# Performance work log

Measured on AMD Instinct MI355X. Metric: run time of the kernel, lower is better.

Reference implementation:

```python
import jax, jax.numpy as jnp
import numpy as np

B, S, H, L = 64, 2048, 1024, 15


def setup_inputs() -> dict:
    key = jax.random.key(0)
    ks = jax.random.split(key, 16)
    x = jax.random.normal(ks[0], (B, S, H), dtype=jnp.float32)
    # valid spans: start in [1, S-40), length in [1, 32)
    s1 = jax.random.randint(ks[1], (B,), 1, S - 40)
    l1 = jax.random.randint(ks[2], (B,), 1, 32)
    s2 = jax.random.randint(ks[3], (B,), 1, S - 40)
    l2 = jax.random.randint(ks[4], (B,), 1, 32)
    entity_idx = jnp.stack([s1, s1 + l1, s2, s2 + l2], axis=1).astype(jnp.int32)
    sc = 1.0 / np.sqrt(H)
    W_cls = jax.random.normal(ks[5], (H, H), jnp.float32) * sc
    b_cls = jnp.zeros((H,), jnp.float32)
    W_e1 = jax.random.normal(ks[6], (H, H), jnp.float32) * sc
    b_e1 = jnp.zeros((H,), jnp.float32)
    W_e2 = jax.random.normal(ks[7], (H, H), jnp.float32) * sc
    b_e2 = jnp.zeros((H,), jnp.float32)
    W1 = jax.random.normal(ks[8], (3 * H, H), jnp.float32) * (1.0 / np.sqrt(3 * H))
    b1 = jnp.zeros((H,), jnp.float32)
    W2 = jax.random.normal(ks[9], (H, H), jnp.float32) * sc
    b2 = jnp.zeros((H,), jnp.float32)
    Wout = jax.random.normal(ks[10], (H, L), jnp.float32) * sc
    bout = jnp.zeros((L,), jnp.float32)
    return {"x": x, "entity_idx": entity_idx, "W_cls": W_cls, "b_cls": b_cls,
            "W_e1": W_e1, "b_e1": b_e1, "W_e2": W_e2, "b_e2": b_e2,
            "W1": W1, "b1": b1, "W2": W2, "b2": b2, "Wout": Wout, "bout": bout}


def _span_mean(x, start, end):
    # x: [B,S,H]; start,end: [B] int -> masked mean over [start,end)
    pos = jnp.arange(x.shape[1])[None, :]  # [1,S]
    mask = ((pos >= start[:, None]) & (pos < end[:, None])).astype(x.dtype)  # [B,S]
    cnt = jnp.maximum(mask.sum(axis=1, keepdims=True), 1.0)  # [B,1]
    return jnp.einsum('bs,bsh->bh', mask, x) / cnt


def reference(x, entity_idx, W_cls, b_cls, W_e1, b_e1, W_e2, b_e2,
              W1, b1, W2, b2, Wout, bout):
    subj = _span_mean(x, entity_idx[:, 0], entity_idx[:, 1])  # [B,H]
    obj = _span_mean(x, entity_idx[:, 2], entity_idx[:, 3])   # [B,H]
    x0 = jnp.tanh(x[:, 0, :]) @ W_cls + b_cls
    e1 = jnp.tanh(subj) @ W_e1 + b_e1
    e2 = jnp.tanh(obj) @ W_e2 + b_e2
    h = jnp.concatenate([x0, e1, e2], axis=1)  # [B,3H]
    h = h @ W1 + b1           # dropout is identity at eval
    h = h @ W2 + b2
    out = h @ Wout + bout     # [B,num_labels]
    return out
```

## Files before the change

kernel.cpp:

```cpp
#include <hip/hip_runtime.h>
#include <math.h>

#define BB 64
#define SS 2048
#define HH 1024
#define LL 15

__global__ void span_tanh_kernel(const float* __restrict__ x,
                                 const int* __restrict__ eidx,
                                 float* __restrict__ t_cat,
                                 float* __restrict__ h_cat,
                                 float* __restrict__ h1,
                                 float* __restrict__ h2) {
  int b = blockIdx.x;
  int part = blockIdx.y;
  int tid = threadIdx.x;
  int h4 = tid * 4;
  const float* xb = x + (size_t)b * SS * HH;
  float* tb = t_cat + (size_t)b * 3 * HH;
  const float4 zero4 = {0.f, 0.f, 0.f, 0.f};

  if (part == 0) {
    float4* z = (float4*)(h_cat + (size_t)b * 3 * HH);
    z[tid] = zero4; z[tid + 256] = zero4; z[tid + 512] = zero4;

    int s1 = eidx[b * 4 + 0], e1 = eidx[b * 4 + 1];
    float c1 = (float)max(e1 - s1, 1);
    float4 v0 = *(const float4*)&xb[h4];
    float4 a = zero4;
    for (int s = s1; s < e1; ++s) {
      float4 v = *(const float4*)&xb[(size_t)s * HH + h4];
      a.x += v.x; a.y += v.y; a.z += v.z; a.w += v.w;
    }
    float4 o0 = {tanhf(v0.x), tanhf(v0.y), tanhf(v0.z), tanhf(v0.w)};
    *(float4*)&tb[h4] = o0;
    float4 o1 = {tanhf(a.x / c1), tanhf(a.y / c1), tanhf(a.z / c1), tanhf(a.w / c1)};
    *(float4*)&tb[HH + h4] = o1;
  } else {
    ((float4*)(h1 + (size_t)b * HH))[tid] = zero4;
    ((float4*)(h2 + (size_t)b * HH))[tid] = zero4;

    int s2 = eidx[b * 4 + 2], e2 = eidx[b * 4 + 3];
    float c2 = (float)max(e2 - s2, 1);
    float4 a = zero4;
    for (int s = s2; s < e2; ++s) {
      float4 v = *(const float4*)&xb[(size_t)s * HH + h4];
      a.x += v.x; a.y += v.y; a.z += v.z; a.w += v.w;
    }
    float4 o2 = {tanhf(a.x / c2), tanhf(a.y / c2), tanhf(a.z / c2), tanhf(a.w / c2)};
    *(float4*)&tb[2 * HH + h4] = o2;
  }
}

#define LSTR 68
__device__ __forceinline__ void gemm_tile_body(
    const float* __restrict__ A, int lda,
    const float* __restrict__ W, int ldw,
    const float* __restrict__ bias,
    float* __restrict__ C, int ldc,
    int k0, int kend, int j0, bool addBias) {
  __shared__ float As[32 * LSTR];
  __shared__ float Ws[32 * LSTR];
  int tid = threadIdx.x;
  int tx = tid & 15, ty = tid >> 4;

  float4 aReg[2], wReg[2];
  int aRow[2], aKq[2], wRow[2], wCq[2];
#pragma unroll
  for (int i = 0; i < 2; ++i) {
    int idx = tid + i * 256;
    aRow[i] = idx & 63; aKq[i] = idx >> 6;
    wRow[i] = idx >> 4; wCq[i] = idx & 15;
  }

  auto loadRegs = [&](int kb) {
#pragma unroll
    for (int i = 0; i < 2; ++i) {
      aReg[i] = *(const float4*)&A[(size_t)aRow[i] * lda + kb + 4 * aKq[i]];
      wReg[i] = *(const float4*)&W[(size_t)(kb + wRow[i]) * ldw + j0 + 4 * wCq[i]];
    }
  };

  float acc[4][4] = {{0.f}};
  loadRegs(k0);
  for (int kb = k0; kb < kend; kb += 32) {
#pragma unroll
    for (int i = 0; i < 2; ++i) {
      float av[4] = {aReg[i].x, aReg[i].y, aReg[i].z, aReg[i].w};
#pragma unroll
      for (int j = 0; j < 4; ++j) As[(4 * aKq[i] + j) * LSTR + aRow[i]] = av[j];
      *(float4*)&Ws[wRow[i] * LSTR + 4 * wCq[i]] = wReg[i];
    }
    __syncthreads();
    if (kb + 32 < kend) loadRegs(kb + 32);
#pragma unroll
    for (int kk = 0; kk < 32; ++kk) {
      float4 a4 = *(const float4*)&As[kk * LSTR + ty * 4];
      float4 w4 = *(const float4*)&Ws[kk * LSTR + tx * 4];
      float a[4] = {a4.x, a4.y, a4.z, a4.w};
      float w[4] = {w4.x, w4.y, w4.z, w4.w};
#pragma unroll
      for (int i = 0; i < 4; ++i)
#pragma unroll
        for (int j = 0; j < 4; ++j) acc[i][j] += a[i] * w[j];
    }
    __syncthreads();
  }
#pragma unroll
  for (int i = 0; i < 4; ++i) {
    int r = ty * 4 + i;
#pragma unroll
    for (int j = 0; j < 4; ++j) {
      int c = j0 + tx * 4 + j;
      float v = acc[i][j];
      if (addBias) v += bias[c];
      atomicAdd(&C[(size_t)r * ldc + c], v);
    }
  }
}

__global__ void gemm_bd_kernel(const float* __restrict__ t_cat,
                               const float* __restrict__ Wc, const float* __restrict__ bc,
                               const float* __restrict__ We1, const float* __restrict__ be1,
                               const float* __restrict__ We2, const float* __restrict__ be2,
                               float* __restrict__ h_cat, int Kchunk) {
  int z = blockIdx.z;
  const float* W = (z == 0) ? Wc : ((z == 1) ? We1 : We2);
  const float* bias = (z == 0) ? bc : ((z == 1) ? be1 : be2);
  const float* A = t_cat + z * HH;
  float* C = h_cat + z * HH;
  int k0 = blockIdx.y * Kchunk;
  gemm_tile_body(A, 3 * HH, W, HH, bias, C, 3 * HH,
                 k0, k0 + Kchunk, blockIdx.x * 64, blockIdx.y == 0);
}

__global__ void gemm_kernel(const float* __restrict__ A, int lda,
                            const float* __restrict__ W, int ldw,
                            const float* __restrict__ bias,
                            float* __restrict__ C, int ldc, int Kchunk) {
  int k0 = blockIdx.y * Kchunk;
  gemm_tile_body(A, lda, W, ldw, bias, C, ldc,
                 k0, k0 + Kchunk, blockIdx.x * 64, blockIdx.y == 0);
}

__global__ void out_kernel(const float* __restrict__ h2,
                           const float* __restrict__ Wout,
                           const float* __restrict__ bout,
                           float* __restrict__ out) {
  int tid = threadIdx.x;
  int lane = tid & 63;
  int idx = blockIdx.x * 4 + (tid >> 6);
  int b = idx / LL, l = idx % LL;
  const float* h = h2 + (size_t)b * HH;
  float acc = 0.f;
#pragma unroll
  for (int w = 0; w < 4; ++w) {
    int k0 = (w * 64 + lane) * 4;
    float4 h4 = *(const float4*)&h[k0];
    acc += h4.x * Wout[(size_t)(k0 + 0) * LL + l];
    acc += h4.y * Wout[(size_t)(k0 + 1) * LL + l];
    acc += h4.z * Wout[(size_t)(k0 + 2) * LL + l];
    acc += h4.w * Wout[(size_t)(k0 + 3) * LL + l];
  }
#pragma unroll
  for (int off = 32; off > 0; off >>= 1) acc += __shfl_down(acc, off, 64);
  if (lane == 0) out[idx] = acc + bout[l];
}

extern "C" void kernel_launch(void* const* d_in, const int* in_sizes, int n_in,
                              void* d_out, int out_size, void* d_ws, size_t ws_size,
                              hipStream_t stream) {
  const float* x     = (const float*)d_in[0];
  const int*   eidx  = (const int*)d_in[1];
  const float* W_cls = (const float*)d_in[2];
  const float* b_cls = (const float*)d_in[3];
  const float* W_e1  = (const float*)d_in[4];
  const float* b_e1  = (const float*)d_in[5];
  const float* W_e2  = (const float*)d_in[6];
  const float* b_e2  = (const float*)d_in[7];
  const float* W1    = (const float*)d_in[8];
  const float* b1    = (const float*)d_in[9];
  const float* W2    = (const float*)d_in[10];
  const float* b2    = (const float*)d_in[11];
  const float* Wout  = (const float*)d_in[12];
  const float* bout  = (const float*)d_in[13];
  float* out = (float*)d_out;

  float* ws    = (float*)d_ws;
  float* t_cat = ws;
  float* h_cat = t_cat + BB * 3 * HH;
  float* h1    = h_cat + BB * 3 * HH;
  float* h2    = h1 + BB * HH;

  span_tanh_kernel<<<dim3(BB, 2), 256, 0, stream>>>(x, eidx, t_cat, h_cat, h1, h2);

  gemm_bd_kernel<<<dim3(16, 8, 3), 256, 0, stream>>>(
      t_cat, W_cls, b_cls, W_e1, b_e1, W_e2, b_e2, h_cat, 128);

  gemm_kernel<<<dim3(16, 24, 1), 256, 0, stream>>>(h_cat, 3 * HH, W1, HH, b1, h1, HH, 128);

  gemm_kernel<<<dim3(16, 16, 1), 256, 0, stream>>>(h1, HH, W2, HH, b2, h2, HH, 64);

  out_kernel<<<dim3(240), 256, 0, stream>>>(h2, Wout, bout, out);
}
```

Measured before the change: 718.7 us.

## Fuse all stages into one cooperative persistent kernel with grid syncs

Replaces five separate kernel launches with a single cooperative kernel of 512 blocks that runs the span pooling, three GEMM stages and the output projection, separated by grid-wide syncs. The split-K factors change: the W1 GEMM now uses 32 K-chunks of 96 and the W2 GEMM 32 chunks of 32, so more blocks run in those stages. The aim is to remove launch gaps and make better use of the GPU for the small GEMMs. In exchange it adds grid.sync overhead, more atomicAdd contention from the finer split-K, and a cooperative launch whose return value is never checked.

```diff
diff --git a/kernel.cpp b/kernel.cpp
--- a/kernel.cpp
+++ b/kernel.cpp
@@ -1,58 +1,16 @@
 #include <hip/hip_runtime.h>
+#include <hip/hip_cooperative_groups.h>
 #include <math.h>
 
 #define BB 64
 #define SS 2048
 #define HH 1024
 #define LL 15
-
-__global__ void span_tanh_kernel(const float* __restrict__ x,
-                                 const int* __restrict__ eidx,
-                                 float* __restrict__ t_cat,
-                                 float* __restrict__ h_cat,
-                                 float* __restrict__ h1,
-                                 float* __restrict__ h2) {
-  int b = blockIdx.x;
-  int part = blockIdx.y;
-  int tid = threadIdx.x;
-  int h4 = tid * 4;
-  const float* xb = x + (size_t)b * SS * HH;
-  float* tb = t_cat + (size_t)b * 3 * HH;
-  const float4 zero4 = {0.f, 0.f, 0.f, 0.f};
-
-  if (part == 0) {
-    float4* z = (float4*)(h_cat + (size_t)b * 3 * HH);
-    z[tid] = zero4; z[tid + 256] = zero4; z[tid + 512] = zero4;
-
-    int s1 = eidx[b * 4 + 0], e1 = eidx[b * 4 + 1];
-    float c1 = (float)max(e1 - s1, 1);
-    float4 v0 = *(const float4*)&xb[h4];
-    float4 a = zero4;
-    for (int s = s1; s < e1; ++s) {
-      float4 v = *(const float4*)&xb[(size_t)s * HH + h4];
-      a.x += v.x; a.y += v.y; a.z += v.z; a.w += v.w;
-    }
-    float4 o0 = {tanhf(v0.x), tanhf(v0.y), tanhf(v0.z), tanhf(v0.w)};
-    *(float4*)&tb[h4] = o0;
-    float4 o1 = {tanhf(a.x / c1), tanhf(a.y / c1), tanhf(a.z / c1), tanhf(a.w / c1)};
-    *(float4*)&tb[HH + h4] = o1;
-  } else {
-    ((float4*)(h1 + (size_t)b * HH))[tid] = zero4;
-    ((float4*)(h2 + (size_t)b * HH))[tid] = zero4;
-
-    int s2 = eidx[b * 4 + 2], e2 = eidx[b * 4 + 3];
-    float c2 = (float)max(e2 - s2, 1);
-    float4 a = zero4;
-    for (int s = s2; s < e2; ++s) {
-      float4 v = *(const float4*)&xb[(size_t)s * HH + h4];
-      a.x += v.x; a.y += v.y; a.z += v.z; a.w += v.w;
-    }
-    float4 o2 = {tanhf(a.x / c2), tanhf(a.y / c2), tanhf(a.z / c2), tanhf(a.w / c2)};
-    *(float4*)&tb[2 * HH + h4] = o2;
-  }
-}
-
+#define NBLK 512
 #define LSTR 68
+
+namespace cg = cooperative_groups;
+
 __device__ __forceinline__ void gemm_tile_body(
     const float* __restrict__ A, int lda,
     const float* __restrict__ W, int ldw,
@@ -119,52 +77,111 @@
   }
 }
 
-__global__ void gemm_bd_kernel(const float* __restrict__ t_cat,
-                               const float* __restrict__ Wc, const float* __restrict__ bc,
-                               const float* __restrict__ We1, const float* __restrict__ be1,
-                               const float* __restrict__ We2, const float* __restrict__ be2,
-                               float* __restrict__ h_cat, int Kchunk) {
-  int z = blockIdx.z;
-  const float* W = (z == 0) ? Wc : ((z == 1) ? We1 : We2);
-  const float* bias = (z == 0) ? bc : ((z == 1) ? be1 : be2);
-  const float* A = t_cat + z * HH;
-  float* C = h_cat + z * HH;
-  int k0 = blockIdx.y * Kchunk;
-  gemm_tile_body(A, 3 * HH, W, HH, bias, C, 3 * HH,
-                 k0, k0 + Kchunk, blockIdx.x * 64, blockIdx.y == 0);
-}
-
-__global__ void gemm_kernel(const float* __restrict__ A, int lda,
-                            const float* __restrict__ W, int ldw,
-                            const float* __restrict__ bias,
-                            float* __restrict__ C, int ldc, int Kchunk) {
-  int k0 = blockIdx.y * Kchunk;
-  gemm_tile_body(A, lda, W, ldw, bias, C, ldc,
-                 k0, k0 + Kchunk, blockIdx.x * 64, blockIdx.y == 0);
-}
-
-__global__ void out_kernel(const float* __restrict__ h2,
-                           const float* __restrict__ Wout,
-                           const float* __restrict__ bout,
-                           float* __restrict__ out) {
+__global__ void fused_kernel(const float* __restrict__ x,
+                             const int* __restrict__ eidx,
+                             const float* __restrict__ W_cls, const float* __restrict__ b_cls,
+                             const float* __restrict__ W_e1,  const float* __restrict__ b_e1,
+                             const float* __restrict__ W_e2,  const float* __restrict__ b_e2,
+                             const float* __restrict__ W1,    const float* __restrict__ b1,
+                             const float* __restrict__ W2,    const float* __restrict__ b2,
+                             const float* __restrict__ Wout,  const float* __restrict__ bout,
+                             float* __restrict__ out,
+                             float* __restrict__ t_cat,
+                             float* __restrict__ h_cat,
+                             float* __restrict__ h1,
+                             float* __restrict__ h2) {
+  cg::grid_group grid = cg::this_grid();
+  int blk = blockIdx.x;
   int tid = threadIdx.x;
-  int lane = tid & 63;
-  int idx = blockIdx.x * 4 + (tid >> 6);
-  int b = idx / LL, l = idx % LL;
-  const float* h = h2 + (size_t)b * HH;
-  float acc = 0.f;
-#pragma unroll
-  for (int w = 0; w < 4; ++w) {
-    int k0 = (w * 64 + lane) * 4;
-    float4 h4 = *(const float4*)&h[k0];
-    acc += h4.x * Wout[(size_t)(k0 + 0) * LL + l];
-    acc += h4.y * Wout[(size_t)(k0 + 1) * LL + l];
-    acc += h4.z * Wout[(size_t)(k0 + 2) * LL + l];
-    acc += h4.w * Wout[(size_t)(k0 + 3) * LL + l];
-  }
-#pragma unroll
-  for (int off = 32; off > 0; off >>= 1) acc += __shfl_down(acc, off, 64);
-  if (lane == 0) out[idx] = acc + bout[l];
+
+  {
+    const float4 zero4 = {0.f, 0.f, 0.f, 0.f};
+    int zidx = blk * 256 + tid;
+    if (zidx < (BB * 5 * HH) / 4) ((float4*)h_cat)[zidx] = zero4;
+
+    if (blk < 2 * BB) {
+      int b = blk & 63;
+      int part = blk >> 6;
+      int h4 = tid * 4;
+      const float* xb = x + (size_t)b * SS * HH;
+      float* tb = t_cat + (size_t)b * 3 * HH;
+      if (part == 0) {
+        int s1 = eidx[b * 4 + 0], e1 = eidx[b * 4 + 1];
+        float c1 = (float)max(e1 - s1, 1);
+        float4 v0 = *(const float4*)&xb[h4];
+        float4 a = zero4;
+        for (int s = s1; s < e1; ++s) {
+          float4 v = *(const float4*)&xb[(size_t)s * HH + h4];
+          a.x += v.x; a.y += v.y; a.z += v.z; a.w += v.w;
+        }
+        float4 o0 = {tanhf(v0.x), tanhf(v0.y), tanhf(v0.z), tanhf(v0.w)};
+        *(float4*)&tb[h4] = o0;
+        float4 o1 = {tanhf(a.x / c1), tanhf(a.y / c1), tanhf(a.z / c1), tanhf(a.w / c1)};
+        *(float4*)&tb[HH + h4] = o1;
+      } else {
+        int s2 = eidx[b * 4 + 2], e2 = eidx[b * 4 + 3];
+        float c2 = (float)max(e2 - s2, 1);
+        float4 a = zero4;
+        for (int s = s2; s < e2; ++s) {
+          float4 v = *(const float4*)&xb[(size_t)s * HH + h4];
+          a.x += v.x; a.y += v.y; a.z += v.z; a.w += v.w;
+        }
+        float4 o2 = {tanhf(a.x / c2), tanhf(a.y / c2), tanhf(a.z / c2), tanhf(a.w / c2)};
+        *(float4*)&tb[2 * HH + h4] = o2;
+      }
+    }
+  }
+  grid.sync();
+
+  if (blk < 384) {
+    int jcol = blk & 15;
+    int rest = blk >> 4;
+    int ks = rest & 7;
+    int z = rest >> 3;
+    const float* W = (z == 0) ? W_cls : ((z == 1) ? W_e1 : W_e2);
+    const float* bias = (z == 0) ? b_cls : ((z == 1) ? b_e1 : b_e2);
+    gemm_tile_body(t_cat + z * HH, 3 * HH, W, HH, bias, h_cat + z * HH, 3 * HH,
+                   ks * 128, ks * 128 + 128, jcol * 64, ks == 0);
+  }
+  grid.sync();
+
+  {
+    int jcol = blk & 15;
+    int ks = blk >> 4;
+    gemm_tile_body(h_cat, 3 * HH, W1, HH, b1, h1, HH,
+                   ks * 96, ks * 96 + 96, jcol * 64, ks == 0);
+  }
+  grid.sync();
+
+  {
+    int jcol = blk & 15;
+    int ks = blk >> 4;
+    gemm_tile_body(h1, HH, W2, HH, b2, h2, HH,
+                   ks * 32, ks * 32 + 32, jcol * 64, ks == 0);
+  }
+  grid.sync();
+
+  {
+    int lane = tid & 63;
+    int idx = blk * 4 + (tid >> 6);
+    if (idx < BB * LL) {
+      int b = idx / LL, l = idx % LL;
+      const float* h = h2 + (size_t)b * HH;
+      float acc = 0.f;
+#pragma unroll
+      for (int w = 0; w < 4; ++w) {
+        int k0 = (w * 64 + lane) * 4;
+        float4 hv = *(const float4*)&h[k0];
+        acc += hv.x * Wout[(size_t)(k0 + 0) * LL + l];
+        acc += hv.y * Wout[(size_t)(k0 + 1) * LL + l];
+        acc += hv.z * Wout[(size_t)(k0 + 2) * LL + l];
+        acc += hv.w * Wout[(size_t)(k0 + 3) * LL + l];
+      }
+#pragma unroll
+      for (int off = 32; off > 0; off >>= 1) acc += __shfl_down(acc, off, 64);
+      if (lane == 0) out[idx] = acc + bout[l];
+    }
+  }
 }
 
 extern "C" void kernel_launch(void* const* d_in, const int* in_sizes, int n_in,
@@ -192,14 +209,12 @@
   float* h1    = h_cat + BB * 3 * HH;
   float* h2    = h1 + BB * HH;
 
-  span_tanh_kernel<<<dim3(BB, 2), 256, 0, stream>>>(x, eidx, t_cat, h_cat, h1, h2);
-
-  gemm_bd_kernel<<<dim3(16, 8, 3), 256, 0, stream>>>(
-      t_cat, W_cls, b_cls, W_e1, b_e1, W_e2, b_e2, h_cat, 128);
-
-  gemm_kernel<<<dim3(16, 24, 1), 256, 0, stream>>>(h_cat, 3 * HH, W1, HH, b1, h1, HH, 128);
-
-  gemm_kernel<<<dim3(16, 16, 1), 256, 0, stream>>>(h1, HH, W2, HH, b2, h2, HH, 64);
-
-  out_kernel<<<dim3(240), 256, 0, stream>>>(h2, Wout, bout, out);
+  void* args[] = {
+      (void*)&x, (void*)&eidx,
+      (void*)&W_cls, (void*)&b_cls, (void*)&W_e1, (void*)&b_e1,
+      (void*)&W_e2, (void*)&b_e2, (void*)&W1, (void*)&b1,
+      (void*)&W2, (void*)&b2, (void*)&Wout, (void*)&bout,
+      (void*)&out, (void*)&t_cat, (void*)&h_cat, (void*)&h1, (void*)&h2};
+  hipLaunchCooperativeKernel((void*)fused_kernel, dim3(NBLK), dim3(256),
+                             args, 0, stream);
 }
```

After: 1.022 ms. +42.2%, slower.
